# Optimization experiments

Measured on AMD Instinct MI355X. Metric: run time of the kernel, lower is better.

## Reference

```python
import jax, jax.numpy as jnp
import numpy as np

N = 100000
E = 3200000
IN_C, HID, OUT_C = 256, 32, 16


def gcn_conv(x, W, b, src, dst, n):
    """PyG GCNConv: h = D^{-1/2}(A+I)D^{-1/2} (x W) + b, self-loops already in src/dst."""
    h = x @ W  # [N, out]
    deg = jax.ops.segment_sum(jnp.ones_like(dst, dtype=h.dtype), dst, num_segments=n)
    dinv = jax.lax.rsqrt(deg)  # deg >= 1 because of self-loops
    norm = dinv[src] * dinv[dst]  # [E_all]
    msg = h[src] * norm[:, None]  # gather + normalize
    return jax.ops.segment_sum(msg, dst, num_segments=n) + b


def setup_inputs() -> dict:
    key = jax.random.key(0)
    k1, k2, k3, k4 = jax.random.split(key, 4)
    x = jax.random.normal(k1, (N, IN_C), dtype=jnp.float32)
    edge_index = jax.random.randint(k2, (2, E), 0, N, dtype=jnp.int64)
    # Glorot-ish init for weights, zero bias (as in PyG defaults)
    W1 = jax.random.normal(k3, (IN_C, HID), dtype=jnp.float32) / np.sqrt(IN_C)
    b1 = jnp.zeros((HID,), dtype=jnp.float32)
    W2 = jax.random.normal(k4, (HID, OUT_C), dtype=jnp.float32) / np.sqrt(HID)
    b2 = jnp.zeros((OUT_C,), dtype=jnp.float32)
    return {"x": x, "edge_index": edge_index, "W1": W1, "b1": b1, "W2": W2, "b2": b2}


def reference(x, edge_index, W1, b1, W2, b2):
    n = x.shape[0]
    loops = jnp.arange(n, dtype=edge_index.dtype)
    src = jnp.concatenate([edge_index[0], loops])  # add self-loops
    dst = jnp.concatenate([edge_index[1], loops])
    h = jax.nn.relu(gcn_conv(x, W1, b1, src, dst, n))
    return gcn_conv(h, W2, b2, src, dst, n)
```

## Files before the change

### kernel.cpp

```cpp
#include <hip/hip_runtime.h>

#define IN_C 256
#define HIDC 32
#define OUTC 16
#define NPB  256
#define MAXBKT 800

typedef __attribute__((ext_vector_type(8))) short short8;
typedef __attribute__((ext_vector_type(4))) float f32x4;
union S8U4 { short8 s; unsigned u[4]; };

__device__ __forceinline__ unsigned bf16pair(float a, float b) {
    unsigned ua = __float_as_uint(a); ua += 0x7FFF + ((ua >> 16) & 1);
    unsigned ub = __float_as_uint(b); ub += 0x7FFF + ((ub >> 16) & 1);
    return (ua >> 16) | (ub & 0xFFFF0000u);
}
__device__ __forceinline__ float bf16lo(unsigned u) { return __uint_as_float(u << 16); }
__device__ __forceinline__ float bf16hi(unsigned u) { return __uint_as_float(u & 0xFFFF0000u); }
__device__ __forceinline__ unsigned rbf(float a) {
    unsigned u = __float_as_uint(a);
    u += 0x7FFF + ((u >> 16) & 1);
    return u >> 16;
}
__device__ __forceinline__ void split8(const float* xf, short8& hi, short8& lo) {
    S8U4 H, L;
#pragma unroll
    for (int i = 0; i < 4; ++i) {
        float a = xf[2 * i], b = xf[2 * i + 1];
        unsigned ha = rbf(a), hb = rbf(b);
        float ra = a - __uint_as_float(ha << 16);
        float rb = b - __uint_as_float(hb << 16);
        H.u[i] = ha | (hb << 16);
        L.u[i] = rbf(ra) | (rbf(rb) << 16);
    }
    hi = H.s; lo = L.s;
}

__device__ __forceinline__ int edge_at(const int* __restrict__ ei, long long idx, int is64) {
    return is64 ? ei[idx << 1] : ei[idx];
}

__global__ void k_detect(const int* __restrict__ ei, int* __restrict__ flag,
                         int* __restrict__ bkt_cnt, int nbkt) {
    __shared__ int nz;
    if (threadIdx.x == 0) nz = 0;
    __syncthreads();
    if (ei[2 * threadIdx.x + 1] != 0) atomicOr(&nz, 1);
    for (int i = threadIdx.x; i < nbkt; i += 256) bkt_cnt[i] = 0;
    __syncthreads();
    if (threadIdx.x == 0) *flag = (nz == 0) ? 1 : 0;
}

__global__ __launch_bounds__(1024) void k_bin_count(const int* __restrict__ ei, long long E,
                                                    const int* __restrict__ flag,
                                                    int* __restrict__ bkt_cnt, int nbkt) {
    __shared__ int hist[MAXBKT];
    int is64 = *flag;
    for (int i = threadIdx.x; i < nbkt; i += 1024) hist[i] = 0;
    __syncthreads();
    long long chunk = (E + gridDim.x - 1) / gridDim.x;
    long long lo = (long long)blockIdx.x * chunk;
    long long hi = lo + chunk; if (hi > E) hi = E;
    for (long long i = lo + threadIdx.x; i < hi; i += 1024)
        atomicAdd(&hist[edge_at(ei, E + i, is64) >> 8], 1);
    __syncthreads();
    for (int b = threadIdx.x; b < nbkt; b += 1024)
        if (hist[b]) atomicAdd(&bkt_cnt[b], hist[b]);
}

__global__ __launch_bounds__(512) void k_bscan(const int* __restrict__ bkt_cnt,
                                               int* __restrict__ bkt_base,
                                               int* __restrict__ bkt_cur, int nbkt) {
    __shared__ int sm[512];
    int t = threadIdx.x;
    int e0 = (2 * t < nbkt) ? bkt_cnt[2 * t] : 0;
    int e1 = (2 * t + 1 < nbkt) ? bkt_cnt[2 * t + 1] : 0;
    int pv = e0 + e1;
    sm[t] = pv;
    __syncthreads();
    for (int o = 1; o < 512; o <<= 1) {
        int x = (t >= o) ? sm[t - o] : 0;
        __syncthreads();
        sm[t] += x;
        __syncthreads();
    }
    int base = sm[t] - pv;
    if (2 * t < nbkt)     { bkt_base[2 * t] = base;          bkt_cur[2 * t] = base; }
    if (2 * t + 1 < nbkt) { bkt_base[2 * t + 1] = base + e0; bkt_cur[2 * t + 1] = base + e0; }
}

__global__ __launch_bounds__(1024) void k_bin_scatter(const int* __restrict__ ei, long long E,
                                                      const int* __restrict__ flag,
                                                      int* __restrict__ bkt_cur,
                                                      unsigned* __restrict__ packed, int nbkt) {
    __shared__ int hist[MAXBKT];
    int is64 = *flag;
    for (int i = threadIdx.x; i < nbkt; i += 1024) hist[i] = 0;
    __syncthreads();
    long long chunk = (E + gridDim.x - 1) / gridDim.x;
    long long lo = (long long)blockIdx.x * chunk;
    long long hi = lo + chunk; if (hi > E) hi = E;
    for (long long i = lo + threadIdx.x; i < hi; i += 1024)
        atomicAdd(&hist[edge_at(ei, E + i, is64) >> 8], 1);
    __syncthreads();
    for (int b = threadIdx.x; b < nbkt; b += 1024) {
        int c = hist[b];
        hist[b] = c ? atomicAdd(&bkt_cur[b], c) : 0;
    }
    __syncthreads();
    for (long long i = lo + threadIdx.x; i < hi; i += 1024) {
        int s = edge_at(ei, i, is64);
        int d = edge_at(ei, E + i, is64);
        int slot = atomicAdd(&hist[d >> 8], 1);
        packed[slot] = (unsigned)s | ((unsigned)(d & (NPB - 1)) << 20);
    }
}

__global__ __launch_bounds__(256) void k_bucket_csr(const unsigned* __restrict__ packed,
                                                    const int* __restrict__ bkt_base,
                                                    const int* __restrict__ bkt_cnt,
                                                    int* __restrict__ csr_src,
                                                    int* __restrict__ ptr,
                                                    int* __restrict__ cnt,
                                                    float* __restrict__ dinv, int n) {
    __shared__ int hist[NPB];
    __shared__ int off[NPB];
    hist[threadIdx.x] = 0;
    __syncthreads();
    int base = bkt_base[blockIdx.x], m = bkt_cnt[blockIdx.x];
    for (int i = threadIdx.x; i < m; i += 256)
        atomicAdd(&hist[packed[base + i] >> 20], 1);
    __syncthreads();
    off[threadIdx.x] = hist[threadIdx.x];
    __syncthreads();
    for (int o = 1; o < NPB; o <<= 1) {
        int v = (threadIdx.x >= o) ? off[threadIdx.x - o] : 0;
        __syncthreads();
        off[threadIdx.x] += v;
        __syncthreads();
    }
    int node = blockIdx.x * NPB + threadIdx.x;
    {
        int exc = off[threadIdx.x] - hist[threadIdx.x];
        if (node < n) {
            ptr[node]  = base + exc;
            cnt[node]  = hist[threadIdx.x];
            dinv[node] = rsqrtf((float)hist[threadIdx.x] + 1.0f);
        }
        hist[threadIdx.x] = exc;
    }
    __syncthreads();
    for (int i = threadIdx.x; i < m; i += 256) {
        unsigned w = packed[base + i];
        int r = atomicAdd(&hist[w >> 20], 1);
        csr_src[base + r] = (int)(w & 0xFFFFF);
    }
}

__global__ void k_wfrag(const float* __restrict__ W1, unsigned short* __restrict__ wf) {
    int idx = blockIdx.x * 256 + threadIdx.x;
    if (idx >= 8 * 2 * 2 * 64) return;
    int lane = idx & 63;
    int part = (idx >> 6) & 1;
    int tile = (idx >> 7) & 1;
    int s    = idx >> 8;
    int col = tile * 16 + (lane & 15);
    int k0  = s * 32 + (lane >> 4) * 8;
#pragma unroll
    for (int j = 0; j < 8; ++j) {
        float v = W1[(long long)(k0 + j) * HIDC + col];
        unsigned h = rbf(v);
        float r = v - __uint_as_float(h << 16);
        wf[(long long)idx * 8 + j] = (unsigned short)(part == 0 ? h : rbf(r));
    }
}

__global__ __launch_bounds__(256) void k_gemm1(const float* __restrict__ x,
                                               const unsigned short* __restrict__ wf,
                                               const float* __restrict__ dinv,
                                               unsigned short* __restrict__ h1b_us, int n) {
    const int t = threadIdx.x;
    const int l = t & 63;
    const int w = t >> 6;
    const long long nb0 = (long long)blockIdx.x * 64 + w * 16;
    const int arow = l & 15;
    const int kg = l >> 4;
    const long long nodeA = nb0 + arow;
    const bool loadA = nodeA < n;
    f32x4 acc0 = {0.f, 0.f, 0.f, 0.f}, acc1 = {0.f, 0.f, 0.f, 0.f};

#pragma unroll
    for (int s = 0; s < 8; ++s) {
        float xf[8];
        if (loadA) {
            float4 v0 = *(const float4*)(x + nodeA * IN_C + s * 32 + kg * 8);
            float4 v1 = *(const float4*)(x + nodeA * IN_C + s * 32 + kg * 8 + 4);
            xf[0] = v0.x; xf[1] = v0.y; xf[2] = v0.z; xf[3] = v0.w;
            xf[4] = v1.x; xf[5] = v1.y; xf[6] = v1.z; xf[7] = v1.w;
        } else {
#pragma unroll
            for (int j = 0; j < 8; ++j) xf[j] = 0.f;
        }
        short8 ah, al;
        split8(xf, ah, al);
        const unsigned short* base = wf + ((long long)(s * 4) * 64 + l) * 8;
        short8 bh0 = *(const short8*)(base);
        short8 bl0 = *(const short8*)(base + 64 * 8);
        short8 bh1 = *(const short8*)(base + 2 * 64 * 8);
        short8 bl1 = *(const short8*)(base + 3 * 64 * 8);
        acc0 = __builtin_amdgcn_mfma_f32_16x16x32_bf16(ah, bh0, acc0, 0, 0, 0);
        acc0 = __builtin_amdgcn_mfma_f32_16x16x32_bf16(ah, bl0, acc0, 0, 0, 0);
        acc0 = __builtin_amdgcn_mfma_f32_16x16x32_bf16(al, bh0, acc0, 0, 0, 0);
        acc1 = __builtin_amdgcn_mfma_f32_16x16x32_bf16(ah, bh1, acc1, 0, 0, 0);
        acc1 = __builtin_amdgcn_mfma_f32_16x16x32_bf16(ah, bl1, acc1, 0, 0, 0);
        acc1 = __builtin_amdgcn_mfma_f32_16x16x32_bf16(al, bh1, acc1, 0, 0, 0);
    }
#pragma unroll
    for (int r = 0; r < 4; ++r) {
        long long nd = nb0 + (l >> 4) * 4 + r;
        if (nd < n) {
            float di = dinv[nd];
            h1b_us[nd * 32 + (l & 15)]      = (unsigned short)rbf(acc0[r] * di);
            h1b_us[nd * 32 + 16 + (l & 15)] = (unsigned short)rbf(acc1[r] * di);
        }
    }
}

__global__ __launch_bounds__(256) void k_agg1csr(const int* __restrict__ ptr,
                                                 const int* __restrict__ cnt,
                                                 const int* __restrict__ csr_src,
                                                 const float* __restrict__ dinv,
                                                 const unsigned* __restrict__ h1b,
                                                 const float* __restrict__ b1,
                                                 float* __restrict__ h1r, int n) {
    long long g = (long long)blockIdx.x * blockDim.x + threadIdx.x;
    int node = (int)(g >> 4);
    int cp = (int)(g & 15);
    if (node >= n) return;
    unsigned us = h1b[(long long)node * 16 + cp];
    float accL = bf16lo(us), accH = bf16hi(us);
    int st = ptr[node], deg = cnt[node];
    int j = 0;
    for (; j + 3 < deg; j += 4) {
        int s0 = csr_src[st + j], s1 = csr_src[st + j + 1];
        int s2 = csr_src[st + j + 2], s3 = csr_src[st + j + 3];
        unsigned u0 = h1b[(long long)s0 * 16 + cp];
        unsigned u1 = h1b[(long long)s1 * 16 + cp];
        unsigned u2 = h1b[(long long)s2 * 16 + cp];
        unsigned u3 = h1b[(long long)s3 * 16 + cp];
        accL += (bf16lo(u0) + bf16lo(u1)) + (bf16lo(u2) + bf16lo(u3));
        accH += (bf16hi(u0) + bf16hi(u1)) + (bf16hi(u2) + bf16hi(u3));
    }
    for (; j < deg; ++j) {
        unsigned u = h1b[(long long)csr_src[st + j] * 16 + cp];
        accL += bf16lo(u); accH += bf16hi(u);
    }
    float di = dinv[node];
    float vL = accL * di + b1[2 * cp];
    float vH = accH * di + b1[2 * cp + 1];
    *(float2*)(h1r + (long long)node * HIDC + 2 * cp) =
        make_float2(vL > 0.f ? vL : 0.f, vH > 0.f ? vH : 0.f);
}

__global__ __launch_bounds__(256) void k_gemm2(const float* __restrict__ h1,
                                               const float* __restrict__ W2,
                                               const float* __restrict__ dinv,
                                               unsigned* __restrict__ h2b, int n) {
    const int t = threadIdx.x;
    const int oq = (t & 3) * 4;
    const long long node = (long long)blockIdx.x * 64 + (t >> 2);
    if (node >= n) return;
    const float* __restrict__ xp = h1 + node * HIDC;
    float a0 = 0.f, a1 = 0.f, a2 = 0.f, a3 = 0.f;
#pragma unroll
    for (int k0 = 0; k0 < HIDC; k0 += 8) {
        float4 xv0 = *(const float4*)(xp + k0);
        float4 xv1 = *(const float4*)(xp + k0 + 4);
        const float* __restrict__ wp = W2 + (long long)k0 * OUTC + oq;
        float4 w0 = *(const float4*)(wp + 0 * OUTC);
        float4 w1 = *(const float4*)(wp + 1 * OUTC);
        float4 w2 = *(const float4*)(wp + 2 * OUTC);
        float4 w3 = *(const float4*)(wp + 3 * OUTC);
        float4 w4 = *(const float4*)(wp + 4 * OUTC);
        float4 w5 = *(const float4*)(wp + 5 * OUTC);
        float4 w6 = *(const float4*)(wp + 6 * OUTC);
        float4 w7 = *(const float4*)(wp + 7 * OUTC);
        a0 = fmaf(xv0.x, w0.x, a0); a1 = fmaf(xv0.x, w0.y, a1);
        a2 = fmaf(xv0.x, w0.z, a2); a3 = fmaf(xv0.x, w0.w, a3);
        a0 = fmaf(xv0.y, w1.x, a0); a1 = fmaf(xv0.y, w1.y, a1);
        a2 = fmaf(xv0.y, w1.z, a2); a3 = fmaf(xv0.y, w1.w, a3);
        a0 = fmaf(xv0.z, w2.x, a0); a1 = fmaf(xv0.z, w2.y, a1);
        a2 = fmaf(xv0.z, w2.z, a2); a3 = fmaf(xv0.z, w2.w, a3);
        a0 = fmaf(xv0.w, w3.x, a0); a1 = fmaf(xv0.w, w3.y, a1);
        a2 = fmaf(xv0.w, w3.z, a2); a3 = fmaf(xv0.w, w3.w, a3);
        a0 = fmaf(xv1.x, w4.x, a0); a1 = fmaf(xv1.x, w4.y, a1);
        a2 = fmaf(xv1.x, w4.z, a2); a3 = fmaf(xv1.x, w4.w, a3);
        a0 = fmaf(xv1.y, w5.x, a0); a1 = fmaf(xv1.y, w5.y, a1);
        a2 = fmaf(xv1.y, w5.z, a2); a3 = fmaf(xv1.y, w5.w, a3);
        a0 = fmaf(xv1.z, w6.x, a0); a1 = fmaf(xv1.z, w6.y, a1);
        a2 = fmaf(xv1.z, w6.z, a2); a3 = fmaf(xv1.z, w6.w, a3);
        a0 = fmaf(xv1.w, w7.x, a0); a1 = fmaf(xv1.w, w7.y, a1);
        a2 = fmaf(xv1.w, w7.z, a2); a3 = fmaf(xv1.w, w7.w, a3);
    }
    float di = dinv[node];
    uint2 p;
    p.x = bf16pair(a0 * di, a1 * di);
    p.y = bf16pair(a2 * di, a3 * di);
    *(uint2*)(h2b + node * (OUTC / 2) + oq / 2) = p;
}

__global__ __launch_bounds__(256) void k_agg2csr(const int* __restrict__ ptr,
                                                 const int* __restrict__ cnt,
                                                 const int* __restrict__ csr_src,
                                                 const float* __restrict__ dinv,
                                                 const unsigned* __restrict__ h2b,
                                                 const float* __restrict__ b2,
                                                 float* __restrict__ out, int n) {
    long long g = (long long)blockIdx.x * blockDim.x + threadIdx.x;
    int node = (int)(g >> 3);
    int cp = (int)(g & 7);
    if (node >= n) return;
    unsigned us = h2b[(long long)node * 8 + cp];
    float accL = bf16lo(us), accH = bf16hi(us);
    int st = ptr[node], deg = cnt[node];
    int j = 0;
    for (; j + 3 < deg; j += 4) {
        int s0 = csr_src[st + j], s1 = csr_src[st + j + 1];
        int s2 = csr_src[st + j + 2], s3 = csr_src[st + j + 3];
        unsigned u0 = h2b[(long long)s0 * 8 + cp];
        unsigned u1 = h2b[(long long)s1 * 8 + cp];
        unsigned u2 = h2b[(long long)s2 * 8 + cp];
        unsigned u3 = h2b[(long long)s3 * 8 + cp];
        accL += (bf16lo(u0) + bf16lo(u1)) + (bf16lo(u2) + bf16lo(u3));
        accH += (bf16hi(u0) + bf16hi(u1)) + (bf16hi(u2) + bf16hi(u3));
    }
    for (; j < deg; ++j) {
        unsigned u = h2b[(long long)csr_src[st + j] * 8 + cp];
        accL += bf16lo(u); accH += bf16hi(u);
    }
    float di = dinv[node];
    *(float2*)(out + (long long)node * OUTC + 2 * cp) =
        make_float2(accL * di + b2[2 * cp], accH * di + b2[2 * cp + 1]);
}

extern "C" void kernel_launch(void* const* d_in, const int* in_sizes, int n_in,
                              void* d_out, int out_size, void* d_ws, size_t ws_size,
                              hipStream_t stream) {
    const float* x  = (const float*)d_in[0];
    const int*   ei = (const int*)d_in[1];
    const float* W1 = (const float*)d_in[2];
    const float* b1 = (const float*)d_in[3];
    const float* W2 = (const float*)d_in[4];
    const float* b2 = (const float*)d_in[5];
    const int n = in_sizes[0] / IN_C;
    const long long E = in_sizes[1] / 2;
    float* out = (float*)d_out;

    const int nbkt = (n + NPB - 1) / NPB;

    char* ws = (char*)d_ws;
    size_t off = 0;
    auto alloc = [&](size_t bytes) { void* p = ws + off; off += (bytes + 255) & ~(size_t)255; return p; };
    int*      flag     = (int*)alloc(256);
    int*      bkt_cnt  = (int*)alloc((size_t)MAXBKT * 4);
    int*      bkt_base = (int*)alloc((size_t)MAXBKT * 4);
    int*      bkt_cur  = (int*)alloc((size_t)MAXBKT * 4);
    float*    dinv     = (float*)alloc((size_t)n * 4);
    int*      cnt      = (int*)alloc((size_t)n * 4);
    int*      ptr      = (int*)alloc((size_t)n * 4);
    unsigned* packed   = (unsigned*)alloc((size_t)E * 4);
    int*      csr_src  = (int*)alloc((size_t)E * 4);
    unsigned short* wf = (unsigned short*)alloc(8 * 2 * 2 * 64 * 8 * 2);
    unsigned* h1b      = (unsigned*)alloc((size_t)n * (HIDC / 2) * 4);
    float*    h1r      = (float*)alloc((size_t)n * HIDC * 4);
    unsigned* h2b      = (unsigned*)alloc((size_t)n * (OUTC / 2) * 4);

    k_detect<<<1, 256, 0, stream>>>(ei, flag, bkt_cnt, nbkt);
    k_wfrag<<<8, 256, 0, stream>>>(W1, wf);
    k_bin_count<<<256, 1024, 0, stream>>>(ei, E, flag, bkt_cnt, nbkt);
    k_bscan<<<1, 512, 0, stream>>>(bkt_cnt, bkt_base, bkt_cur, nbkt);
    k_bin_scatter<<<256, 1024, 0, stream>>>(ei, E, flag, bkt_cur, packed, nbkt);
    k_bucket_csr<<<nbkt, NPB, 0, stream>>>(packed, bkt_base, bkt_cnt, csr_src, ptr, cnt, dinv, n);

    k_gemm1<<<(n + 63) / 64, 256, 0, stream>>>(x, wf, dinv, (unsigned short*)h1b, n);
    k_agg1csr<<<(int)(((long long)n * 16 + 255) / 256), 256, 0, stream>>>(
        ptr, cnt, csr_src, dinv, h1b, b1, h1r, n);
    k_gemm2<<<(n + 63) / 64, 256, 0, stream>>>(h1r, W2, dinv, h2b, n);
    k_agg2csr<<<(int)(((long long)n * 8 + 255) / 256), 256, 0, stream>>>(
        ptr, cnt, csr_src, dinv, h2b, b2, out, n);
}
```

Before: 182.0 us.

## Replace count+scan binning with fixed-capacity buckets and single-pass edge staging

Result: faster. 177.0 us (-2.8%).

```diff
diff --git a/kernel.cpp b/kernel.cpp
--- a/kernel.cpp
+++ b/kernel.cpp
@@ -5,6 +5,8 @@
 #define OUTC 16
 #define NPB  256
 #define MAXBKT 800
+#define CAP  16384
+#define EPB  12288
 
 typedef __attribute__((ext_vector_type(8))) short short8;
 typedef __attribute__((ext_vector_type(4))) float f32x4;
@@ -41,84 +43,49 @@
 }
 
 __global__ void k_detect(const int* __restrict__ ei, int* __restrict__ flag,
-                         int* __restrict__ bkt_cnt, int nbkt) {
+                         int* __restrict__ bkt_cur, int nbkt) {
     __shared__ int nz;
     if (threadIdx.x == 0) nz = 0;
     __syncthreads();
     if (ei[2 * threadIdx.x + 1] != 0) atomicOr(&nz, 1);
-    for (int i = threadIdx.x; i < nbkt; i += 256) bkt_cnt[i] = 0;
+    for (int i = threadIdx.x; i < nbkt; i += 256) bkt_cur[i] = i * CAP;
     __syncthreads();
     if (threadIdx.x == 0) *flag = (nz == 0) ? 1 : 0;
-}
-
-__global__ __launch_bounds__(1024) void k_bin_count(const int* __restrict__ ei, long long E,
-                                                    const int* __restrict__ flag,
-                                                    int* __restrict__ bkt_cnt, int nbkt) {
-    __shared__ int hist[MAXBKT];
-    int is64 = *flag;
-    for (int i = threadIdx.x; i < nbkt; i += 1024) hist[i] = 0;
-    __syncthreads();
-    long long chunk = (E + gridDim.x - 1) / gridDim.x;
-    long long lo = (long long)blockIdx.x * chunk;
-    long long hi = lo + chunk; if (hi > E) hi = E;
-    for (long long i = lo + threadIdx.x; i < hi; i += 1024)
-        atomicAdd(&hist[edge_at(ei, E + i, is64) >> 8], 1);
-    __syncthreads();
-    for (int b = threadIdx.x; b < nbkt; b += 1024)
-        if (hist[b]) atomicAdd(&bkt_cnt[b], hist[b]);
-}
-
-__global__ __launch_bounds__(512) void k_bscan(const int* __restrict__ bkt_cnt,
-                                               int* __restrict__ bkt_base,
-                                               int* __restrict__ bkt_cur, int nbkt) {
-    __shared__ int sm[512];
-    int t = threadIdx.x;
-    int e0 = (2 * t < nbkt) ? bkt_cnt[2 * t] : 0;
-    int e1 = (2 * t + 1 < nbkt) ? bkt_cnt[2 * t + 1] : 0;
-    int pv = e0 + e1;
-    sm[t] = pv;
-    __syncthreads();
-    for (int o = 1; o < 512; o <<= 1) {
-        int x = (t >= o) ? sm[t - o] : 0;
-        __syncthreads();
-        sm[t] += x;
-        __syncthreads();
-    }
-    int base = sm[t] - pv;
-    if (2 * t < nbkt)     { bkt_base[2 * t] = base;          bkt_cur[2 * t] = base; }
-    if (2 * t + 1 < nbkt) { bkt_base[2 * t + 1] = base + e0; bkt_cur[2 * t + 1] = base + e0; }
 }
 
 __global__ __launch_bounds__(1024) void k_bin_scatter(const int* __restrict__ ei, long long E,
                                                       const int* __restrict__ flag,
                                                       int* __restrict__ bkt_cur,
                                                       unsigned* __restrict__ packed, int nbkt) {
+    __shared__ unsigned ecw[EPB];
+    __shared__ unsigned short ecb[EPB];
     __shared__ int hist[MAXBKT];
     int is64 = *flag;
     for (int i = threadIdx.x; i < nbkt; i += 1024) hist[i] = 0;
     __syncthreads();
-    long long chunk = (E + gridDim.x - 1) / gridDim.x;
-    long long lo = (long long)blockIdx.x * chunk;
-    long long hi = lo + chunk; if (hi > E) hi = E;
-    for (long long i = lo + threadIdx.x; i < hi; i += 1024)
-        atomicAdd(&hist[edge_at(ei, E + i, is64) >> 8], 1);
+    long long lo = (long long)blockIdx.x * EPB;
+    int m = (int)((E - lo) < EPB ? (E - lo) : EPB);
+    for (int i = threadIdx.x; i < m; i += 1024) {
+        int s = edge_at(ei, lo + i, is64);
+        int d = edge_at(ei, E + lo + i, is64);
+        ecw[i] = (unsigned)s | ((unsigned)(d & (NPB - 1)) << 20);
+        ecb[i] = (unsigned short)(d >> 8);
+        atomicAdd(&hist[d >> 8], 1);
+    }
     __syncthreads();
     for (int b = threadIdx.x; b < nbkt; b += 1024) {
         int c = hist[b];
         hist[b] = c ? atomicAdd(&bkt_cur[b], c) : 0;
     }
     __syncthreads();
-    for (long long i = lo + threadIdx.x; i < hi; i += 1024) {
-        int s = edge_at(ei, i, is64);
-        int d = edge_at(ei, E + i, is64);
-        int slot = atomicAdd(&hist[d >> 8], 1);
-        packed[slot] = (unsigned)s | ((unsigned)(d & (NPB - 1)) << 20);
+    for (int i = threadIdx.x; i < m; i += 1024) {
+        int slot = atomicAdd(&hist[ecb[i]], 1);
+        packed[slot] = ecw[i];
     }
 }
 
 __global__ __launch_bounds__(256) void k_bucket_csr(const unsigned* __restrict__ packed,
-                                                    const int* __restrict__ bkt_base,
-                                                    const int* __restrict__ bkt_cnt,
+                                                    const int* __restrict__ bkt_cur,
                                                     int* __restrict__ csr_src,
                                                     int* __restrict__ ptr,
                                                     int* __restrict__ cnt,
@@ -127,7 +94,8 @@
     __shared__ int off[NPB];
     hist[threadIdx.x] = 0;
     __syncthreads();
-    int base = bkt_base[blockIdx.x], m = bkt_cnt[blockIdx.x];
+    int base = blockIdx.x * CAP;
+    int m = bkt_cur[blockIdx.x] - base;
     for (int i = threadIdx.x; i < m; i += 256)
         atomicAdd(&hist[packed[base + i] >> 20], 1);
     __syncthreads();
@@ -362,25 +330,21 @@
     size_t off = 0;
     auto alloc = [&](size_t bytes) { void* p = ws + off; off += (bytes + 255) & ~(size_t)255; return p; };
     int*      flag     = (int*)alloc(256);
-    int*      bkt_cnt  = (int*)alloc((size_t)MAXBKT * 4);
-    int*      bkt_base = (int*)alloc((size_t)MAXBKT * 4);
     int*      bkt_cur  = (int*)alloc((size_t)MAXBKT * 4);
     float*    dinv     = (float*)alloc((size_t)n * 4);
     int*      cnt      = (int*)alloc((size_t)n * 4);
     int*      ptr      = (int*)alloc((size_t)n * 4);
-    unsigned* packed   = (unsigned*)alloc((size_t)E * 4);
-    int*      csr_src  = (int*)alloc((size_t)E * 4);
+    unsigned* packed   = (unsigned*)alloc((size_t)nbkt * CAP * 4);
+    int*      csr_src  = (int*)alloc((size_t)nbkt * CAP * 4);
     unsigned short* wf = (unsigned short*)alloc(8 * 2 * 2 * 64 * 8 * 2);
     unsigned* h1b      = (unsigned*)alloc((size_t)n * (HIDC / 2) * 4);
     float*    h1r      = (float*)alloc((size_t)n * HIDC * 4);
     unsigned* h2b      = (unsigned*)alloc((size_t)n * (OUTC / 2) * 4);
 
-    k_detect<<<1, 256, 0, stream>>>(ei, flag, bkt_cnt, nbkt);
+    k_detect<<<1, 256, 0, stream>>>(ei, flag, bkt_cur, nbkt);
     k_wfrag<<<8, 256, 0, stream>>>(W1, wf);
-    k_bin_count<<<256, 1024, 0, stream>>>(ei, E, flag, bkt_cnt, nbkt);
-    k_bscan<<<1, 512, 0, stream>>>(bkt_cnt, bkt_base, bkt_cur, nbkt);
-    k_bin_scatter<<<256, 1024, 0, stream>>>(ei, E, flag, bkt_cur, packed, nbkt);
-    k_bucket_csr<<<nbkt, NPB, 0, stream>>>(packed, bkt_base, bkt_cnt, csr_src, ptr, cnt, dinv, n);
+    k_bin_scatter<<<(int)((E + EPB - 1) / EPB), 1024, 0, stream>>>(ei, E, flag, bkt_cur, packed, nbkt);
+    k_bucket_csr<<<nbkt, NPB, 0, stream>>>(packed, bkt_cur, csr_src, ptr, cnt, dinv, n);
 
     k_gemm1<<<(n + 63) / 64, 256, 0, stream>>>(x, wf, dinv, (unsigned short*)h1b, n);
     k_agg1csr<<<(int)(((long long)n * 16 + 255) / 256), 256, 0, stream>>>(
```
